# Performance work log

Measured on AMD Instinct MI355X. Metric: run time of the kernel, lower is better.

The kernel has to match this reference:

```python
import jax, jax.numpy as jnp
import numpy as np
import math

D_INPUT = 1024
D_Q = 1024
D_K = 1024
D_V = 1024
D_MODEL = 1024
B, S = 4, 2048


def setup_inputs() -> dict:
    key = jax.random.key(0)
    ks = jax.random.split(key, 9)
    sc = 0.02
    return {
        "x": jax.random.normal(ks[0], (B, S, D_INPUT), dtype=jnp.float32),
        "wq": jax.random.normal(ks[1], (D_INPUT, D_Q), dtype=jnp.float32) * sc,
        "bq": jnp.zeros((D_Q,), dtype=jnp.float32),
        "wk": jax.random.normal(ks[2], (D_INPUT, D_K), dtype=jnp.float32) * sc,
        "bk": jnp.zeros((D_K,), dtype=jnp.float32),
        "wv": jax.random.normal(ks[3], (D_INPUT, D_V), dtype=jnp.float32) * sc,
        "bv": jnp.zeros((D_V,), dtype=jnp.float32),
        "wp": jax.random.normal(ks[4], (D_V, D_MODEL), dtype=jnp.float32) * sc,
        "bp": jnp.zeros((D_MODEL,), dtype=jnp.float32),
    }


def reference(x, wq, bq, wk, bk, wv, bv, wp, bp):
    scale = math.sqrt(D_K)  # NOTE: original MULTIPLIES by sqrt(d_k)
    q = x @ wq + bq  # [B,S,Dq]
    k = x @ wk + bk  # [B,S,Dk]
    v = x @ wv + bv  # [B,S,Dv]
    scores = jnp.einsum('bsd,btd->bst', q, k) * scale
    p_attn = jax.nn.softmax(scores, axis=-1)
    # dropout: inference mode (training=False) -> identity
    context = jnp.einsum('bst,btd->bsd', p_attn, v)
    output = context @ wp + bp
    return (output, p_attn)
```

## Files before the change

### kernel.cpp

```cpp
#include <hip/hip_runtime.h>

typedef unsigned short u16;
typedef short bf16x8 __attribute__((ext_vector_type(8)));
typedef float floatx4 __attribute__((ext_vector_type(4)));

static __device__ __forceinline__ u16 f2bf(float f) {
  unsigned int u = __float_as_uint(f);
  unsigned int lsb = (u >> 16) & 1u;
  u += 0x7FFFu + lsb;
  return (u16)(u >> 16);
}
static __device__ __forceinline__ float bf2f(u16 u) {
  return __uint_as_float(((unsigned int)u) << 16);
}

static __device__ __forceinline__ void gl_lds16(const u16* g, u16* l) {
  __builtin_amdgcn_global_load_lds(
      (const __attribute__((address_space(1))) void*)g,
      (__attribute__((address_space(3))) void*)l, 16, 0, 0);
}

__global__ __launch_bounds__(256)
void prep_all(const float* __restrict__ wq, const float* __restrict__ wk,
              const float* __restrict__ wv, const float* __restrict__ wp,
              const float* __restrict__ bq, const float* __restrict__ bk,
              const float* __restrict__ x,
              u16* __restrict__ qkThi, u16* __restrict__ qkTlo,
              u16* __restrict__ wvThi, u16* __restrict__ wpThi,
              float* __restrict__ bqk,
              u16* __restrict__ xhi, u16* __restrict__ xlo,
              u16* __restrict__ xThi) {
  __shared__ float t[32][33];
  const int z = blockIdx.z;
  const int tid = threadIdx.x;
  const int lr = tid >> 3;
  const int lc = (tid & 7) * 4;

  if (z == 4) {
    if (blockIdx.y == 0 && blockIdx.x < 8) {
      const int i = blockIdx.x * 256 + tid;
      bqk[i] = (i < 1024) ? bq[i] : bk[i - 1024];
    }
    return;
  }

  if (z >= 5) {
    const int r0 = ((z - 5) * 32 + blockIdx.y) * 32;
    const int c0 = blockIdx.x * 32;
    float4 v = *(const float4*)(x + (size_t)(r0 + lr) * 1024 + c0 + lc);
    float f[4] = {v.x, v.y, v.z, v.w};
    t[lr][lc + 0] = v.x; t[lr][lc + 1] = v.y; t[lr][lc + 2] = v.z; t[lr][lc + 3] = v.w;
    u16 ph[4], pl[4];
#pragma unroll
    for (int j = 0; j < 4; j++) {
      ph[j] = f2bf(f[j]);
      pl[j] = f2bf(f[j] - bf2f(ph[j]));
    }
    const size_t o = (size_t)(r0 + lr) * 1024 + c0 + lc;
    *(uint2*)(xhi + o) = *(uint2*)ph;
    *(uint2*)(xlo + o) = *(uint2*)pl;
    __syncthreads();
    u16 pt[4];
#pragma unroll
    for (int j = 0; j < 4; j++) pt[j] = f2bf(t[lc + j][lr]);
    const int b = r0 >> 11, rt = r0 & 2047;
    *(uint2*)(xThi + (size_t)b * (1024 * 2048) + (size_t)(c0 + lr) * 2048 + rt + lc) =
        *(uint2*)pt;
    return;
  }

  const float* in = (z == 0) ? wq : (z == 1) ? wk : (z == 2) ? wv : wp;
  u16* hi = (z == 2) ? wvThi : (z == 3) ? wpThi : (qkThi + (size_t)z * 1024 * 1024);
  u16* lo = (z == 0) ? qkTlo : (z == 1) ? (qkTlo + 1024 * 1024) : (u16*)nullptr;
  const int want_lo = (z < 2);

  const int r0 = blockIdx.y * 32, c0 = blockIdx.x * 32;
  float4 v = *(const float4*)(in + (size_t)(r0 + lr) * 1024 + c0 + lc);
  t[lr][lc + 0] = v.x; t[lr][lc + 1] = v.y; t[lr][lc + 2] = v.z; t[lr][lc + 3] = v.w;
  __syncthreads();
  u16 ph[4], pl[4];
#pragma unroll
  for (int j = 0; j < 4; j++) {
    float f = t[lc + j][lr];
    ph[j] = f2bf(f);
    if (want_lo) pl[j] = f2bf(f - bf2f(ph[j]));
  }
  const size_t o = (size_t)(c0 + lr) * 1024 + r0 + lc;
  *(uint2*)(hi + o) = *(uint2*)ph;
  if (want_lo) *(uint2*)(lo + o) = *(uint2*)pl;
}

template<int KB, int ASP, int BSP, int OM, int HB>
__global__ __launch_bounds__(256)
void gemm_mfma(const u16* __restrict__ Ahi, const u16* __restrict__ Alo,
               const u16* __restrict__ Bhi, const u16* __restrict__ Blo,
               const float* __restrict__ bias,
               void* __restrict__ C0, void* __restrict__ C1,
               void* __restrict__ C2, void* __restrict__ C3,
               int N, int K, int lda, int ldb, int ldc,
               long long aB, long long bB, long long cB, float scale) {
  constexpr int CM = KB / 8 - 1;
  constexpr int RPI = 512 / KB;
  constexpr int NI = KB / 16;
  constexpr int PL = 128 * KB;
  __shared__ __align__(16) u16 As[(1 + ASP) * PL];
  __shared__ __align__(16) u16 Bs[(1 + BSP) * PL];

  const int bz = blockIdx.z;
  const u16* A0 = Ahi + (size_t)bz * aB;
  const u16* A1 = ASP ? (Alo + (size_t)bz * aB) : (const u16*)nullptr;
  const u16* B0 = Bhi + (size_t)bz * bB;
  const u16* B1 = BSP ? (Blo + (size_t)bz * bB) : (const u16*)nullptr;

  const int m0 = blockIdx.y * 128;
  const int n0 = blockIdx.x * 128;
  const int tid = threadIdx.x;
  const int w = tid >> 6;
  const int L = tid & 63;
  const int rr = L & 15, quad = L >> 4;
  const int wm = (w >> 1) * 64, wn = (w & 1) * 64;

  const int lrow = (KB == 32) ? (L >> 2) : (L >> 3);
  const int c3 = (L & CM) ^ ((L >> 3) & CM);
  const int srow = w * 32 + lrow;
  u16* stA = &As[w * 32 * KB];
  u16* stB = &Bs[w * 32 * KB];
  const u16* gA0 = A0 + (size_t)(m0 + srow) * lda + c3 * 8;
  const u16* gA1 = ASP ? A1 + (size_t)(m0 + srow) * lda + c3 * 8 : (const u16*)nullptr;
  const u16* gB0 = B0 + (size_t)(n0 + srow) * ldb + c3 * 8;
  const u16* gB1 = BSP ? B1 + (size_t)(n0 + srow) * ldb + c3 * 8 : (const u16*)nullptr;

  floatx4 acc[4][4] = {};

  for (int k0 = 0; k0 < K; k0 += KB) {
#pragma unroll
    for (int q = 0; q < NI; q++) {
      gl_lds16(gA0 + k0 + (size_t)q * RPI * lda, stA + q * 512);
      gl_lds16(gB0 + k0 + (size_t)q * RPI * ldb, stB + q * 512);
    }
    if (ASP) {
#pragma unroll
      for (int q = 0; q < NI; q++)
        gl_lds16(gA1 + k0 + (size_t)q * RPI * lda, stA + PL + q * 512);
    }
    if (BSP) {
#pragma unroll
      for (int q = 0; q < NI; q++)
        gl_lds16(gB1 + k0 + (size_t)q * RPI * ldb, stB + PL + q * 512);
    }
    __syncthreads();

#pragma unroll
    for (int s = 0; s < KB / 32; s++) {
      const int pcb = ((KB == 32) ? (quad ^ ((rr >> 1) & 3))
                                  : ((s * 4 + quad) ^ (rr & 7))) * 8;
      bf16x8 a0[4], a1[4], b0[4], b1[4];
#pragma unroll
      for (int i = 0; i < 4; i++) {
        const int arow = wm + i * 16 + rr;
        const int brow = wn + i * 16 + rr;
        a0[i] = *(const bf16x8*)&As[arow * KB + pcb];
        b0[i] = *(const bf16x8*)&Bs[brow * KB + pcb];
        if (ASP) a1[i] = *(const bf16x8*)&As[PL + arow * KB + pcb];
        if (BSP) b1[i] = *(const bf16x8*)&Bs[PL + brow * KB + pcb];
      }
#pragma unroll
      for (int i = 0; i < 4; i++) {
#pragma unroll
        for (int j = 0; j < 4; j++) {
          acc[i][j] = __builtin_amdgcn_mfma_f32_16x16x32_bf16(a0[i], b0[j], acc[i][j], 0, 0, 0);
          if (ASP && BSP) {
            acc[i][j] = __builtin_amdgcn_mfma_f32_16x16x32_bf16(a0[i], b1[j], acc[i][j], 0, 0, 0);
            acc[i][j] = __builtin_amdgcn_mfma_f32_16x16x32_bf16(a1[i], b0[j], acc[i][j], 0, 0, 0);
          }
        }
      }
    }
    __syncthreads();
  }

#pragma unroll
  for (int i = 0; i < 4; i++) {
    const int mbase = m0 + wm + i * 16 + quad * 4;
#pragma unroll
    for (int j = 0; j < 4; j++) {
      const int col = n0 + wn + j * 16 + rr;
      float bvs = 0.f;
      if (HB) bvs = bias[col];
      if (OM == 5) {
        u16* hi; u16* lo;
        if (col < 1024) { hi = (u16*)C0; lo = (u16*)C1; }
        else            { hi = (u16*)C2; lo = (u16*)C3; }
        const int cc = col & 1023;
#pragma unroll
        for (int ii = 0; ii < 4; ii++) {
          const float v = acc[i][j][ii] + bvs;
          const size_t idx = (size_t)(mbase + ii) * 1024 + cc;
          const u16 h = f2bf(v);
          hi[idx] = h;
          lo[idx] = f2bf(v - bf2f(h));
        }
      } else {
        u16* Cb = (u16*)C0 + (size_t)bz * cB;
        float* Cf = (float*)C0 + (size_t)bz * cB;
        u16* Cl = (OM == 1) ? ((u16*)C1 + (size_t)bz * cB) : (u16*)nullptr;
#pragma unroll
        for (int ii = 0; ii < 4; ii++) {
          const float v = acc[i][j][ii] * scale + bvs;
          const size_t idx = (size_t)(mbase + ii) * ldc + col;
          if (OM == 0) {
            Cb[idx] = f2bf(v);
          } else if (OM == 1) {
            const u16 h = f2bf(v);
            Cb[idx] = h;
            Cl[idx] = f2bf(v - bf2f(h));
          } else {
            Cf[idx] = v;
          }
        }
      }
    }
  }
}

template<int OM>
__global__ __launch_bounds__(512, 2)
void gemm8(const u16* __restrict__ Ahi, const u16* __restrict__ Alo,
           const u16* __restrict__ Bhi, const u16* __restrict__ Blo,
           const float* __restrict__ bias,
           void* __restrict__ C0, void* __restrict__ C1,
           void* __restrict__ C2, void* __restrict__ C3,
           long long aB, long long bB, long long cB, float scale) {
  __shared__ __align__(16) u16 As[4 * 8192];
  __shared__ __align__(16) u16 Bs[4 * 8192];

  const int gx = gridDim.x, gy = gridDim.y, gz = gridDim.z;
  const int flat = blockIdx.x + gx * (blockIdx.y + gy * blockIdx.z);
  const int nwg = gx * gy * gz;
  const int lg = (flat & 7) * (nwg >> 3) + (flat >> 3);
  const int bx = lg % gx;
  const int by = (lg / gx) % gy;
  const int bz = lg / (gx * gy);

  const int m0 = by * 256, n0 = bx * 256;
  const u16* pAhi = Ahi + (size_t)bz * aB;
  const u16* pAlo = Alo + (size_t)bz * aB;
  const u16* pBhi = Bhi + (size_t)bz * bB;
  const u16* pBlo = Blo + (size_t)bz * bB;

  const int tid = threadIdx.x;
  const int w = tid >> 6;
  const int L = tid & 63;
  const int rr = L & 15, quad = L >> 4;
  const int wm = (w >> 2) * 128;
  const int wn = (w & 3) * 64;

  const int rbase = w * 16 + (L >> 2);
  const int coff = (((L & 3) ^ ((L >> 3) & 3)) << 3);
  const int arow = (m0 + rbase) * 1024 + coff;
  const int brow = (n0 + rbase) * 1024 + coff;
  u16* const ldA = As + w * 512;
  u16* const ldB = Bs + w * 512;

  const int aoff = ((wm + rr) << 5) + ((quad ^ ((rr >> 1) & 3)) << 3);
  const int boff = ((wn + rr) << 5) + ((quad ^ ((rr >> 1) & 3)) << 3);

  auto stageA = [&](int H) {
    const int kt = H >> 1;
    const u16* src = (kt < 32) ? pAhi : pAlo;
    const int koff = ((kt & 15) << 6) + ((H & 1) << 5);
    const u16* g = src + arow + koff;
    u16* l = ldA + (H & 3) * 8192;
    gl_lds16(g, l);
    gl_lds16(g + 128 * 1024, l + 4096);
  };
  auto stageB = [&](int H) {
    const int kt = H >> 1;
    const u16* src = (kt < 16) ? pBhi : (kt < 32) ? pBlo : pBhi;
    const int koff = ((kt & 15) << 6) + ((H & 1) << 5);
    const u16* g = src + brow + koff;
    u16* l = ldB + (H & 3) * 8192;
    gl_lds16(g, l);
    gl_lds16(g + 128 * 1024, l + 4096);
  };

  floatx4 acc[8][4] = {};
  bf16x8 aE[8], aO[8], b01E[2], b01O[2], b23[2];

#define RD_SET(slot, A_, B_)                                                   \
  {                                                                            \
    const u16* ab_ = As + ((slot) & 3) * 8192 + aoff;                          \
    const u16* bb_ = Bs + ((slot) & 3) * 8192 + boff;                          \
    _Pragma("unroll")                                                          \
    for (int i = 0; i < 8; i++) A_[i] = *(const bf16x8*)(ab_ + i * 512);       \
    B_[0] = *(const bf16x8*)(bb_);                                             \
    B_[1] = *(const bf16x8*)(bb_ + 512);                                       \
  }

#define PAIRX(H, AC, B01C, AN, B01N, SB2, SA3, RDN, VM)                        \
  {                                                                            \
    __builtin_amdgcn_sched_barrier(0);                                         \
    {                                                                          \
      const u16* bb_ = Bs + ((H) & 3) * 8192 + boff;                           \
      b23[0] = *(const bf16x8*)(bb_ + 1024);                                   \
      b23[1] = *(const bf16x8*)(bb_ + 1536);                                   \
    }                                                                          \
    if (SB2) stageB((H) + 2);                                                  \
    __builtin_amdgcn_sched_barrier(0);                                         \
    __builtin_amdgcn_s_setprio(1);                                             \
    _Pragma("unroll")                                                          \
    for (int i = 0; i < 8; i++) {                                              \
      acc[i][0] = __builtin_amdgcn_mfma_f32_16x16x32_bf16(AC[i], B01C[0], acc[i][0], 0, 0, 0); \
      acc[i][1] = __builtin_amdgcn_mfma_f32_16x16x32_bf16(AC[i], B01C[1], acc[i][1], 0, 0, 0); \
    }                                                                          \
    __builtin_amdgcn_s_setprio(0);                                             \
    __builtin_amdgcn_sched_barrier(0);                                         \
    if (RDN) RD_SET((H) + 1, AN, B01N);                                        \
    if (SA3) stageA((H) + 3);                                                  \
    __builtin_amdgcn_sched_barrier(0);                                         \
    __builtin_amdgcn_s_setprio(1);                                             \
    _Pragma("unroll")                                                          \
    for (int i = 0; i < 8; i++) {                                              \
      acc[i][2] = __builtin_amdgcn_mfma_f32_16x16x32_bf16(AC[i], b23[0], acc[i][2], 0, 0, 0); \
      acc[i][3] = __builtin_amdgcn_mfma_f32_16x16x32_bf16(AC[i], b23[1], acc[i][3], 0, 0, 0); \
    }                                                                          \
    __builtin_amdgcn_s_setprio(0);                                             \
    if ((VM) == 2) asm volatile("s_waitcnt vmcnt(2)");                         \
    else if ((VM) == 0) asm volatile("s_waitcnt vmcnt(0)");                    \
    __builtin_amdgcn_s_barrier();                                              \
  }

  stageA(0); stageB(0); stageA(1); stageB(1); stageA(2);
  asm volatile("s_waitcnt vmcnt(2)");
  __builtin_amdgcn_s_barrier();
  RD_SET(0, aE, b01E);

  for (int H = 0; H < 92; H += 2) {
    PAIRX(H,     aE, b01E, aO, b01O, true, true, true, 2);
    PAIRX(H + 1, aO, b01O, aE, b01E, true, true, true, 2);
  }
  PAIRX(92, aE, b01E, aO, b01O, true,  true,  true,  2);
  PAIRX(93, aO, b01O, aE, b01E, true,  false, true,  0);
  PAIRX(94, aE, b01E, aO, b01O, false, false, true,  -1);
  PAIRX(95, aO, b01O, aE, b01E, false, false, false, -1);
#undef PAIRX
#undef RD_SET

#pragma unroll
  for (int i = 0; i < 8; i++) {
    const int mb = m0 + wm + i * 16 + quad * 4;
#pragma unroll
    for (int j = 0; j < 4; j++) {
      const int col = n0 + wn + j * 16 + rr;
      if (OM == 5) {
        u16* hi; u16* lo;
        if (col < 1024) { hi = (u16*)C0; lo = (u16*)C1; }
        else            { hi = (u16*)C2; lo = (u16*)C3; }
        const int cc = col & 1023;
        const float bvs = bias[col];
#pragma unroll
        for (int ii = 0; ii < 4; ii++) {
          const float v = acc[i][j][ii] + bvs;
          const size_t idx = (size_t)(mb + ii) * 1024 + cc;
          const u16 h = f2bf(v);
          hi[idx] = h;
          lo[idx] = f2bf(v - bf2f(h));
        }
      } else {
        float* Cf = (float*)C0 + (size_t)bz * cB;
#pragma unroll
        for (int ii = 0; ii < 4; ii++)
          Cf[(size_t)(mb + ii) * 2048 + col] = acc[i][j][ii] * scale;
      }
    }
  }
}

__global__ __launch_bounds__(256)
void softmax_rows(float* __restrict__ S, u16* __restrict__ Pb) {
  const int row = blockIdx.x;
  float* s = S + (size_t)row * 2048;
  const int tid = threadIdx.x;
  const int w = tid >> 6;
  __shared__ float redm[4];
  __shared__ float reds[4];

  float v[8];
  float mx = -1e30f;
#pragma unroll
  for (int i = 0; i < 8; i++) {
    v[i] = s[tid + 256 * i];
    mx = fmaxf(mx, v[i]);
  }
#pragma unroll
  for (int o = 32; o > 0; o >>= 1) mx = fmaxf(mx, __shfl_xor(mx, o, 64));
  if ((tid & 63) == 0) redm[w] = mx;
  __syncthreads();
  mx = fmaxf(fmaxf(redm[0], redm[1]), fmaxf(redm[2], redm[3]));

  float sum = 0.f;
#pragma unroll
  for (int i = 0; i < 8; i++) {
    v[i] = __expf(v[i] - mx);
    sum += v[i];
  }
#pragma unroll
  for (int o = 32; o > 0; o >>= 1) sum += __shfl_xor(sum, o, 64);
  if ((tid & 63) == 0) reds[w] = sum;
  __syncthreads();
  sum = reds[0] + reds[1] + reds[2] + reds[3];
  const float rs = 1.0f / sum;
#pragma unroll
  for (int i = 0; i < 8; i++) {
    const float p = v[i] * rs;
    s[tid + 256 * i] = p;
    Pb[(size_t)row * 2048 + tid + 256 * i] = f2bf(p);
  }
}

extern "C" void kernel_launch(void* const* d_in, const int* in_sizes, int n_in,
                              void* d_out, int out_size, void* d_ws, size_t ws_size,
                              hipStream_t stream) {
  const float* x  = (const float*)d_in[0];
  const float* wq = (const float*)d_in[1];
  const float* bq = (const float*)d_in[2];
  const float* wk = (const float*)d_in[3];
  const float* bk = (const float*)d_in[4];
  const float* wv = (const float*)d_in[5];
  const float* bv = (const float*)d_in[6];
  const float* wp = (const float*)d_in[7];
  const float* bp = (const float*)d_in[8];

  const size_t MB = 1024 * 1024;
  char* ws = (char*)d_ws;
  u16* qkThi = (u16*)(ws + 0 * MB);
  u16* qkTlo = (u16*)(ws + 4 * MB);
  u16* wvThi = (u16*)(ws + 8 * MB);
  u16* wpThi = (u16*)(ws + 10 * MB);
  float* bqk = (float*)(ws + 12 * MB);
  u16* xhi   = (u16*)(ws + 13 * MB);
  u16* xlo   = (u16*)(ws + 29 * MB);
  u16* qhi   = (u16*)(ws + 45 * MB);
  u16* qlo   = (u16*)(ws + 61 * MB);
  u16* khi   = (u16*)(ws + 77 * MB);
  u16* klo   = (u16*)(ws + 93 * MB);
  u16* xThi  = (u16*)(ws + 109 * MB);
  u16* pbf   = khi;
  u16* px    = qhi;
  u16* ctx   = qlo;

  float* outp = (float*)d_out;
  float* scf  = (float*)d_out + 8388608;

  const dim3 blk(256);

  prep_all<<<dim3(32, 32, 13), blk, 0, stream>>>(
      wq, wk, wv, wp, bq, bk, x, qkThi, qkTlo, wvThi, wpThi, bqk, xhi, xlo, xThi);

  gemm8<5><<<dim3(8, 32, 1), dim3(512), 0, stream>>>(
      xhi, xlo, qkThi, qkTlo, bqk, qhi, qlo, khi, klo, 0, 0, 0, 1.0f);

  gemm8<2><<<dim3(8, 8, 4), dim3(512), 0, stream>>>(
      qhi, qlo, khi, klo, nullptr, scf, nullptr, nullptr, nullptr,
      2048LL * 1024, 2048LL * 1024, 2048LL * 2048, 32.0f);

  softmax_rows<<<dim3(8192), blk, 0, stream>>>(scf, pbf);

  gemm_mfma<64, 0, 0, 0, 0><<<dim3(8, 16, 4), blk, 0, stream>>>(
      pbf, nullptr, xThi, nullptr, nullptr, px, nullptr, nullptr, nullptr,
      1024, 2048, 2048, 2048, 1024,
      2048LL * 2048, 1024LL * 2048, 2048LL * 1024, 1.0f);

  gemm_mfma<64, 0, 0, 0, 1><<<dim3(8, 64, 1), blk, 0, stream>>>(
      px, nullptr, wvThi, nullptr, bv, ctx, nullptr, nullptr, nullptr,
      1024, 1024, 1024, 1024, 1024, 0, 0, 0, 1.0f);

  gemm_mfma<64, 0, 0, 2, 1><<<dim3(8, 64, 1), blk, 0, stream>>>(
      ctx, nullptr, wpThi, nullptr, bp, outp, nullptr, nullptr, nullptr,
      1024, 1024, 1024, 1024, 1024, 0, 0, 0, 1.0f);
}
```

Baseline: 436.8 us.

## Generalize pipelined gemm8 kernel and use it for the P·X and projection GEMMs

Templates the pipelined 512-thread gemm8 kernel on tile height, split-precision mode, output mode and bias, and passes leading dimensions and the half-step count as runtime arguments. The simpler 256-thread gemm_mfma kernel is removed, and the three remaining bf16 GEMMs (P·X, the V projection, the output projection) now run through gemm8 with 128x256 tiles. The aim is to give these GEMMs the deeper LDS prefetch pipeline, priority-scheduled MFMA blocks and grid swizzle that the QK GEMMs already use. The cost is fewer, larger workgroups: the two 1024x1024 GEMMs drop to 256 blocks, which may underfill the GPU.

After: 439.0 us. Within noise of the previous version (+0.5%).

```diff
diff --git a/kernel.cpp b/kernel.cpp
--- a/kernel.cpp
+++ b/kernel.cpp
@@ -90,148 +90,19 @@
   if (want_lo) *(uint2*)(lo + o) = *(uint2*)pl;
 }
 
-template<int KB, int ASP, int BSP, int OM, int HB>
-__global__ __launch_bounds__(256)
-void gemm_mfma(const u16* __restrict__ Ahi, const u16* __restrict__ Alo,
-               const u16* __restrict__ Bhi, const u16* __restrict__ Blo,
-               const float* __restrict__ bias,
-               void* __restrict__ C0, void* __restrict__ C1,
-               void* __restrict__ C2, void* __restrict__ C3,
-               int N, int K, int lda, int ldb, int ldc,
-               long long aB, long long bB, long long cB, float scale) {
-  constexpr int CM = KB / 8 - 1;
-  constexpr int RPI = 512 / KB;
-  constexpr int NI = KB / 16;
-  constexpr int PL = 128 * KB;
-  __shared__ __align__(16) u16 As[(1 + ASP) * PL];
-  __shared__ __align__(16) u16 Bs[(1 + BSP) * PL];
-
-  const int bz = blockIdx.z;
-  const u16* A0 = Ahi + (size_t)bz * aB;
-  const u16* A1 = ASP ? (Alo + (size_t)bz * aB) : (const u16*)nullptr;
-  const u16* B0 = Bhi + (size_t)bz * bB;
-  const u16* B1 = BSP ? (Blo + (size_t)bz * bB) : (const u16*)nullptr;
-
-  const int m0 = blockIdx.y * 128;
-  const int n0 = blockIdx.x * 128;
-  const int tid = threadIdx.x;
-  const int w = tid >> 6;
-  const int L = tid & 63;
-  const int rr = L & 15, quad = L >> 4;
-  const int wm = (w >> 1) * 64, wn = (w & 1) * 64;
-
-  const int lrow = (KB == 32) ? (L >> 2) : (L >> 3);
-  const int c3 = (L & CM) ^ ((L >> 3) & CM);
-  const int srow = w * 32 + lrow;
-  u16* stA = &As[w * 32 * KB];
-  u16* stB = &Bs[w * 32 * KB];
-  const u16* gA0 = A0 + (size_t)(m0 + srow) * lda + c3 * 8;
-  const u16* gA1 = ASP ? A1 + (size_t)(m0 + srow) * lda + c3 * 8 : (const u16*)nullptr;
-  const u16* gB0 = B0 + (size_t)(n0 + srow) * ldb + c3 * 8;
-  const u16* gB1 = BSP ? B1 + (size_t)(n0 + srow) * ldb + c3 * 8 : (const u16*)nullptr;
-
-  floatx4 acc[4][4] = {};
-
-  for (int k0 = 0; k0 < K; k0 += KB) {
-#pragma unroll
-    for (int q = 0; q < NI; q++) {
-      gl_lds16(gA0 + k0 + (size_t)q * RPI * lda, stA + q * 512);
-      gl_lds16(gB0 + k0 + (size_t)q * RPI * ldb, stB + q * 512);
-    }
-    if (ASP) {
-#pragma unroll
-      for (int q = 0; q < NI; q++)
-        gl_lds16(gA1 + k0 + (size_t)q * RPI * lda, stA + PL + q * 512);
-    }
-    if (BSP) {
-#pragma unroll
-      for (int q = 0; q < NI; q++)
-        gl_lds16(gB1 + k0 + (size_t)q * RPI * ldb, stB + PL + q * 512);
-    }
-    __syncthreads();
-
-#pragma unroll
-    for (int s = 0; s < KB / 32; s++) {
-      const int pcb = ((KB == 32) ? (quad ^ ((rr >> 1) & 3))
-                                  : ((s * 4 + quad) ^ (rr & 7))) * 8;
-      bf16x8 a0[4], a1[4], b0[4], b1[4];
-#pragma unroll
-      for (int i = 0; i < 4; i++) {
-        const int arow = wm + i * 16 + rr;
-        const int brow = wn + i * 16 + rr;
-        a0[i] = *(const bf16x8*)&As[arow * KB + pcb];
-        b0[i] = *(const bf16x8*)&Bs[brow * KB + pcb];
-        if (ASP) a1[i] = *(const bf16x8*)&As[PL + arow * KB + pcb];
-        if (BSP) b1[i] = *(const bf16x8*)&Bs[PL + brow * KB + pcb];
-      }
-#pragma unroll
-      for (int i = 0; i < 4; i++) {
-#pragma unroll
-        for (int j = 0; j < 4; j++) {
-          acc[i][j] = __builtin_amdgcn_mfma_f32_16x16x32_bf16(a0[i], b0[j], acc[i][j], 0, 0, 0);
-          if (ASP && BSP) {
-            acc[i][j] = __builtin_amdgcn_mfma_f32_16x16x32_bf16(a0[i], b1[j], acc[i][j], 0, 0, 0);
-            acc[i][j] = __builtin_amdgcn_mfma_f32_16x16x32_bf16(a1[i], b0[j], acc[i][j], 0, 0, 0);
-          }
-        }
-      }
-    }
-    __syncthreads();
-  }
-
-#pragma unroll
-  for (int i = 0; i < 4; i++) {
-    const int mbase = m0 + wm + i * 16 + quad * 4;
-#pragma unroll
-    for (int j = 0; j < 4; j++) {
-      const int col = n0 + wn + j * 16 + rr;
-      float bvs = 0.f;
-      if (HB) bvs = bias[col];
-      if (OM == 5) {
-        u16* hi; u16* lo;
-        if (col < 1024) { hi = (u16*)C0; lo = (u16*)C1; }
-        else            { hi = (u16*)C2; lo = (u16*)C3; }
-        const int cc = col & 1023;
-#pragma unroll
-        for (int ii = 0; ii < 4; ii++) {
-          const float v = acc[i][j][ii] + bvs;
-          const size_t idx = (size_t)(mbase + ii) * 1024 + cc;
-          const u16 h = f2bf(v);
-          hi[idx] = h;
-          lo[idx] = f2bf(v - bf2f(h));
-        }
-      } else {
-        u16* Cb = (u16*)C0 + (size_t)bz * cB;
-        float* Cf = (float*)C0 + (size_t)bz * cB;
-        u16* Cl = (OM == 1) ? ((u16*)C1 + (size_t)bz * cB) : (u16*)nullptr;
-#pragma unroll
-        for (int ii = 0; ii < 4; ii++) {
-          const float v = acc[i][j][ii] * scale + bvs;
-          const size_t idx = (size_t)(mbase + ii) * ldc + col;
-          if (OM == 0) {
-            Cb[idx] = f2bf(v);
-          } else if (OM == 1) {
-            const u16 h = f2bf(v);
-            Cb[idx] = h;
-            Cl[idx] = f2bf(v - bf2f(h));
-          } else {
-            Cf[idx] = v;
-          }
-        }
-      }
-    }
-  }
-}
-
-template<int OM>
+template<int BM, int SPLIT, int OM, int HB>
 __global__ __launch_bounds__(512, 2)
 void gemm8(const u16* __restrict__ Ahi, const u16* __restrict__ Alo,
            const u16* __restrict__ Bhi, const u16* __restrict__ Blo,
            const float* __restrict__ bias,
            void* __restrict__ C0, void* __restrict__ C1,
            void* __restrict__ C2, void* __restrict__ C3,
+           int lda, int ldb, int ldc, int NP,
            long long aB, long long bB, long long cB, float scale) {
-  __shared__ __align__(16) u16 As[4 * 8192];
+  constexpr int AF = BM / 32;
+  constexpr int ASLOT = BM * 32;
+  constexpr int VMS = BM / 128;
+  __shared__ __align__(16) u16 As[4 * ASLOT];
   __shared__ __align__(16) u16 Bs[4 * 8192];
 
   const int gx = gridDim.x, gy = gridDim.y, gz = gridDim.z;
@@ -242,23 +113,23 @@
   const int by = (lg / gx) % gy;
   const int bz = lg / (gx * gy);
 
-  const int m0 = by * 256, n0 = bx * 256;
+  const int m0 = by * BM, n0 = bx * 256;
   const u16* pAhi = Ahi + (size_t)bz * aB;
-  const u16* pAlo = Alo + (size_t)bz * aB;
+  const u16* pAlo = SPLIT ? (Alo + (size_t)bz * aB) : (const u16*)nullptr;
   const u16* pBhi = Bhi + (size_t)bz * bB;
-  const u16* pBlo = Blo + (size_t)bz * bB;
+  const u16* pBlo = SPLIT ? (Blo + (size_t)bz * bB) : (const u16*)nullptr;
 
   const int tid = threadIdx.x;
   const int w = tid >> 6;
   const int L = tid & 63;
   const int rr = L & 15, quad = L >> 4;
-  const int wm = (w >> 2) * 128;
+  const int wm = (w >> 2) * (BM / 2);
   const int wn = (w & 3) * 64;
 
   const int rbase = w * 16 + (L >> 2);
   const int coff = (((L & 3) ^ ((L >> 3) & 3)) << 3);
-  const int arow = (m0 + rbase) * 1024 + coff;
-  const int brow = (n0 + rbase) * 1024 + coff;
+  const size_t arow = (size_t)(m0 + rbase) * lda + coff;
+  const size_t brow = (size_t)(n0 + rbase) * ldb + coff;
   u16* const ldA = As + w * 512;
   u16* const ldB = Bs + w * 512;
 
@@ -266,33 +137,47 @@
   const int boff = ((wn + rr) << 5) + ((quad ^ ((rr >> 1) & 3)) << 3);
 
   auto stageA = [&](int H) {
-    const int kt = H >> 1;
-    const u16* src = (kt < 32) ? pAhi : pAlo;
-    const int koff = ((kt & 15) << 6) + ((H & 1) << 5);
+    const u16* src;
+    int koff;
+    if (SPLIT) {
+      const int kt = H >> 1;
+      src = (kt < 32) ? pAhi : pAlo;
+      koff = ((kt & 15) << 6) + ((H & 1) << 5);
+    } else {
+      src = pAhi;
+      koff = H << 5;
+    }
     const u16* g = src + arow + koff;
-    u16* l = ldA + (H & 3) * 8192;
+    u16* l = ldA + (H & 3) * ASLOT;
     gl_lds16(g, l);
-    gl_lds16(g + 128 * 1024, l + 4096);
+    if (BM == 256) gl_lds16(g + (size_t)128 * lda, l + 4096);
   };
   auto stageB = [&](int H) {
-    const int kt = H >> 1;
-    const u16* src = (kt < 16) ? pBhi : (kt < 32) ? pBlo : pBhi;
-    const int koff = ((kt & 15) << 6) + ((H & 1) << 5);
+    const u16* src;
+    int koff;
+    if (SPLIT) {
+      const int kt = H >> 1;
+      src = (kt < 16) ? pBhi : (kt < 32) ? pBlo : pBhi;
+      koff = ((kt & 15) << 6) + ((H & 1) << 5);
+    } else {
+      src = pBhi;
+      koff = H << 5;
+    }
     const u16* g = src + brow + koff;
     u16* l = ldB + (H & 3) * 8192;
     gl_lds16(g, l);
-    gl_lds16(g + 128 * 1024, l + 4096);
+    gl_lds16(g + (size_t)128 * ldb, l + 4096);
   };
 
-  floatx4 acc[8][4] = {};
-  bf16x8 aE[8], aO[8], b01E[2], b01O[2], b23[2];
+  floatx4 acc[AF][4] = {};
+  bf16x8 aE[AF], aO[AF], b01E[2], b01O[2], b23[2];
 
 #define RD_SET(slot, A_, B_)                                                   \
   {                                                                            \
-    const u16* ab_ = As + ((slot) & 3) * 8192 + aoff;                          \
+    const u16* ab_ = As + ((slot) & 3) * ASLOT + aoff;                         \
     const u16* bb_ = Bs + ((slot) & 3) * 8192 + boff;                          \
     _Pragma("unroll")                                                          \
-    for (int i = 0; i < 8; i++) A_[i] = *(const bf16x8*)(ab_ + i * 512);       \
+    for (int i = 0; i < AF; i++) A_[i] = *(const bf16x8*)(ab_ + i * 512);      \
     B_[0] = *(const bf16x8*)(bb_);                                             \
     B_[1] = *(const bf16x8*)(bb_ + 512);                                       \
   }
@@ -309,7 +194,7 @@
     __builtin_amdgcn_sched_barrier(0);                                         \
     __builtin_amdgcn_s_setprio(1);                                             \
     _Pragma("unroll")                                                          \
-    for (int i = 0; i < 8; i++) {                                              \
+    for (int i = 0; i < AF; i++) {                                             \
       acc[i][0] = __builtin_amdgcn_mfma_f32_16x16x32_bf16(AC[i], B01C[0], acc[i][0], 0, 0, 0); \
       acc[i][1] = __builtin_amdgcn_mfma_f32_16x16x32_bf16(AC[i], B01C[1], acc[i][1], 0, 0, 0); \
     }                                                                          \
@@ -320,44 +205,50 @@
     __builtin_amdgcn_sched_barrier(0);                                         \
     __builtin_amdgcn_s_setprio(1);                                             \
     _Pragma("unroll")                                                          \
-    for (int i = 0; i < 8; i++) {                                              \
+    for (int i = 0; i < AF; i++) {                                             \
       acc[i][2] = __builtin_amdgcn_mfma_f32_16x16x32_bf16(AC[i], b23[0], acc[i][2], 0, 0, 0); \
       acc[i][3] = __builtin_amdgcn_mfma_f32_16x16x32_bf16(AC[i], b23[1], acc[i][3], 0, 0, 0); \
     }                                                                          \
     __builtin_amdgcn_s_setprio(0);                                             \
     if ((VM) == 2) asm volatile("s_waitcnt vmcnt(2)");                         \
+    else if ((VM) == 1) asm volatile("s_waitcnt vmcnt(1)");                    \
     else if ((VM) == 0) asm volatile("s_waitcnt vmcnt(0)");                    \
     __builtin_amdgcn_s_barrier();                                              \
   }
 
   stageA(0); stageB(0); stageA(1); stageB(1); stageA(2);
-  asm volatile("s_waitcnt vmcnt(2)");
+  if (VMS == 2) asm volatile("s_waitcnt vmcnt(2)");
+  else          asm volatile("s_waitcnt vmcnt(1)");
   __builtin_amdgcn_s_barrier();
   RD_SET(0, aE, b01E);
 
-  for (int H = 0; H < 92; H += 2) {
-    PAIRX(H,     aE, b01E, aO, b01O, true, true, true, 2);
-    PAIRX(H + 1, aO, b01O, aE, b01E, true, true, true, 2);
-  }
-  PAIRX(92, aE, b01E, aO, b01O, true,  true,  true,  2);
-  PAIRX(93, aO, b01O, aE, b01E, true,  false, true,  0);
-  PAIRX(94, aE, b01E, aO, b01O, false, false, true,  -1);
-  PAIRX(95, aO, b01O, aE, b01E, false, false, false, -1);
+  for (int H = 0; H + 4 < NP; H += 2) {
+    PAIRX(H,     aE, b01E, aO, b01O, true, true, true, VMS);
+    PAIRX(H + 1, aO, b01O, aE, b01E, true, true, true, VMS);
+  }
+  {
+    const int T = NP - 4;
+    PAIRX(T,     aE, b01E, aO, b01O, true,  true,  true,  VMS);
+    PAIRX(T + 1, aO, b01O, aE, b01E, true,  false, true,  0);
+    PAIRX(T + 2, aE, b01E, aO, b01O, false, false, true,  -1);
+    PAIRX(T + 3, aO, b01O, aE, b01E, false, false, false, -1);
+  }
 #undef PAIRX
 #undef RD_SET
 
 #pragma unroll
-  for (int i = 0; i < 8; i++) {
+  for (int i = 0; i < AF; i++) {
     const int mb = m0 + wm + i * 16 + quad * 4;
 #pragma unroll
     for (int j = 0; j < 4; j++) {
       const int col = n0 + wn + j * 16 + rr;
+      float bvs = 0.f;
+      if (HB) bvs = bias[col];
       if (OM == 5) {
         u16* hi; u16* lo;
         if (col < 1024) { hi = (u16*)C0; lo = (u16*)C1; }
         else            { hi = (u16*)C2; lo = (u16*)C3; }
         const int cc = col & 1023;
-        const float bvs = bias[col];
 #pragma unroll
         for (int ii = 0; ii < 4; ii++) {
           const float v = acc[i][j][ii] + bvs;
@@ -366,11 +257,18 @@
           hi[idx] = h;
           lo[idx] = f2bf(v - bf2f(h));
         }
+      } else if (OM == 0) {
+        u16* Cb = (u16*)C0 + (size_t)bz * cB;
+#pragma unroll
+        for (int ii = 0; ii < 4; ii++) {
+          const float v = acc[i][j][ii] * scale + bvs;
+          Cb[(size_t)(mb + ii) * ldc + col] = f2bf(v);
+        }
       } else {
         float* Cf = (float*)C0 + (size_t)bz * cB;
 #pragma unroll
         for (int ii = 0; ii < 4; ii++)
-          Cf[(size_t)(mb + ii) * 2048 + col] = acc[i][j][ii] * scale;
+          Cf[(size_t)(mb + ii) * ldc + col] = acc[i][j][ii] * scale + bvs;
       }
     }
   }
@@ -452,30 +350,28 @@
   float* outp = (float*)d_out;
   float* scf  = (float*)d_out + 8388608;
 
-  const dim3 blk(256);
-
-  prep_all<<<dim3(32, 32, 13), blk, 0, stream>>>(
+  prep_all<<<dim3(32, 32, 13), dim3(256), 0, stream>>>(
       wq, wk, wv, wp, bq, bk, x, qkThi, qkTlo, wvThi, wpThi, bqk, xhi, xlo, xThi);
 
-  gemm8<5><<<dim3(8, 32, 1), dim3(512), 0, stream>>>(
-      xhi, xlo, qkThi, qkTlo, bqk, qhi, qlo, khi, klo, 0, 0, 0, 1.0f);
-
-  gemm8<2><<<dim3(8, 8, 4), dim3(512), 0, stream>>>(
+  gemm8<256, 1, 5, 1><<<dim3(8, 32, 1), dim3(512), 0, stream>>>(
+      xhi, xlo, qkThi, qkTlo, bqk, qhi, qlo, khi, klo,
+      1024, 1024, 1024, 96, 0, 0, 0, 1.0f);
+
+  gemm8<256, 1, 2, 0><<<dim3(8, 8, 4), dim3(512), 0, stream>>>(
       qhi, qlo, khi, klo, nullptr, scf, nullptr, nullptr, nullptr,
-      2048LL * 1024, 2048LL * 1024, 2048LL * 2048, 32.0f);
-
-  softmax_rows<<<dim3(8192), blk, 0, stream>>>(scf, pbf);
-
-  gemm_mfma<64, 0, 0, 0, 0><<<dim3(8, 16, 4), blk, 0, stream>>>(
+      1024, 1024, 2048, 96, 2048LL * 1024, 2048LL * 1024, 2048LL * 2048, 32.0f);
+
+  softmax_rows<<<dim3(8192), dim3(256), 0, stream>>>(scf, pbf);
+
+  gemm8<128, 0, 0, 0><<<dim3(4, 16, 4), dim3(512), 0, stream>>>(
       pbf, nullptr, xThi, nullptr, nullptr, px, nullptr, nullptr, nullptr,
-      1024, 2048, 2048, 2048, 1024,
-      2048LL * 2048, 1024LL * 2048, 2048LL * 1024, 1.0f);
-
-  gemm_mfma<64, 0, 0, 0, 1><<<dim3(8, 64, 1), blk, 0, stream>>>(
+      2048, 2048, 1024, 64, 2048LL * 2048, 1024LL * 2048, 2048LL * 1024, 1.0f);
+
+  gemm8<128, 0, 0, 1><<<dim3(4, 64, 1), dim3(512), 0, stream>>>(
       px, nullptr, wvThi, nullptr, bv, ctx, nullptr, nullptr, nullptr,
-      1024, 1024, 1024, 1024, 1024, 0, 0, 0, 1.0f);
-
-  gemm_mfma<64, 0, 0, 2, 1><<<dim3(8, 64, 1), blk, 0, stream>>>(
+      1024, 1024, 1024, 32, 0, 0, 0, 1.0f);
+
+  gemm8<128, 0, 2, 1><<<dim3(4, 64, 1), dim3(512), 0, stream>>>(
       ctx, nullptr, wpThi, nullptr, bp, outp, nullptr, nullptr, nullptr,
-      1024, 1024, 1024, 1024, 1024, 0, 0, 0, 1.0f);
-}
+      1024, 1024, 1024, 32, 0, 0, 0, 1.0f);
+}
```
